# Performance work log

Hardware: AMD Instinct MI355X
Metric: run time of the kernel (lower is better)

Reference implementation:

```python
import jax, jax.numpy as jnp
import numpy as np

T, B, H, N2 = 4096, 2, 2048, 8  # seq_len, batch, embed_dim, ndim//2 complex modes


def setup_inputs() -> dict:
    key = jax.random.key(0)
    k1, k2, k3, k4, k5 = jax.random.split(key, 5)
    x = jax.random.normal(k1, (T, B, H), dtype=jnp.float32)
    D_param = jax.random.normal(k2, (H,), dtype=jnp.float32)
    # dt log-uniform in [1e-3, 1e-1] (standard S4D init)
    u = jax.random.uniform(k3, (H,), dtype=jnp.float32)
    log_dt = u * (jnp.log(0.1) - jnp.log(0.001)) + jnp.log(0.001)
    # S4D-Lin init: A = -1/2 + i*pi*n
    A_real_log = jnp.full((H, N2), jnp.log(0.5), dtype=jnp.float32)
    A_imag = jnp.broadcast_to(np.pi * jnp.arange(N2, dtype=jnp.float32), (H, N2))
    C_re = jax.random.normal(k4, (H, N2), dtype=jnp.float32)
    C_im = jax.random.normal(k5, (H, N2), dtype=jnp.float32)
    return {"x": x, "D_param": D_param, "log_dt": log_dt,
            "A_real_log": A_real_log, "A_imag": A_imag,
            "C_re": C_re, "C_im": C_im}


def _s4d_kernel(log_dt, A_real_log, A_imag, C_re, C_im, L):
    # Diagonal SSM (S4D, ZOH-style) convolution kernel, shape (H, L)
    dt = jnp.exp(log_dt)[:, None]                      # (H, 1)
    A = -jnp.exp(A_real_log) + 1j * A_imag             # (H, N2) complex64
    dtA = A * dt                                       # (H, N2)
    C = (C_re + 1j * C_im) * (jnp.exp(dtA) - 1.0) / A  # discretized C
    vander = jnp.exp(dtA[:, :, None] * jnp.arange(L))  # (H, N2, L)
    return 2.0 * jnp.einsum('hn,hnl->hl', C, vander).real


def reference(x, D_param, log_dt, A_real_log, A_imag, C_re, C_im):
    seq_len = x.shape[0]
    residual = x * D_param                     # (T, B, H)
    xb = jnp.transpose(x, (1, 2, 0))           # (B, H, T)
    k = _s4d_kernel(log_dt, A_real_log, A_imag, C_re, C_im, seq_len)  # (H, T)
    n = 2 * seq_len
    k_f = jnp.fft.rfft(k, n=n)                 # (H, T+1) complex
    x_f = jnp.fft.rfft(xb, n=n)                # (B, H, T+1)
    out = jnp.fft.irfft(x_f * k_f, n=n)[..., :seq_len]  # (B, H, T)
    return jnp.transpose(out, (2, 0, 1)) + residual      # (T, B, H)
```

## Files before the change

kernel.cpp:

```cpp
#include <hip/hip_runtime.h>

#define T_LEN 4096
#define B_SZ  2
#define H_SZ  2048
#define NM    8
#define BH    (B_SZ * H_SZ)


template <int LC>
__global__ void __launch_bounds__(256, 4)
k1_chunk_end(const float* __restrict__ x,
             const float* __restrict__ log_dt,
             const float* __restrict__ Arl,
             const float* __restrict__ Aimp,
             float2* __restrict__ states) {
    int g = blockIdx.x * blockDim.x + threadIdx.x;
    int h = g % H_SZ;
    int b = (g / H_SZ) % B_SZ;
    int c = g / BH;

    float dt = __expf(log_dt[h]);
    float wr[NM], wi[NM];
#pragma unroll
    for (int n = 0; n < NM; ++n) {
        float ar  = -__expf(Arl[h * NM + n]);
        float ai  = Aimp[h * NM + n];
        float er  = __expf(ar * dt);
        float ang = ai * dt;
        wr[n] = er * __cosf(ang);
        wi[n] = er * __sinf(ang);
    }

    float sr[NM], si[NM];
#pragma unroll
    for (int n = 0; n < NM; ++n) { sr[n] = 0.f; si[n] = 0.f; }

    const float* xp = x + (size_t)c * LC * BH + b * H_SZ + h;

    constexpr int BT = 8;
    float buf[BT], nxt[BT];
#pragma unroll
    for (int i = 0; i < BT; ++i) buf[i] = xp[(size_t)i * BH];

#pragma unroll
    for (int tb = 0; tb < LC / BT; ++tb) {
        if (tb + 1 < LC / BT) {
#pragma unroll
            for (int i = 0; i < BT; ++i)
                nxt[i] = xp[(size_t)((tb + 1) * BT + i) * BH];
        }
#pragma unroll
        for (int i = 0; i < BT; ++i) {
            float xv = buf[i];
#pragma unroll
            for (int n = 0; n < NM; ++n) {
                float nsr = fmaf(wr[n], sr[n], fmaf(-wi[n], si[n], xv));
                float nsi = fmaf(wr[n], si[n], wi[n] * sr[n]);
                sr[n] = nsr; si[n] = nsi;
            }
        }
#pragma unroll
        for (int i = 0; i < BT; ++i) buf[i] = nxt[i];
    }

    float2* st = states + (size_t)(c * B_SZ + b) * NM * H_SZ + h;
#pragma unroll
    for (int n = 0; n < NM; ++n) st[(size_t)n * H_SZ] = make_float2(sr[n], si[n]);
}

template <int CC, int LC>
__global__ void __launch_bounds__(256, 4)
k2_carry_scan(const float* __restrict__ log_dt,
              const float* __restrict__ Arl,
              const float* __restrict__ Aimp,
              float2* __restrict__ states) {
    int g = blockIdx.x * blockDim.x + threadIdx.x;
    int h = g % H_SZ;
    int n = (g / H_SZ) % NM;
    int b = g / (H_SZ * NM);

    float dt  = __expf(log_dt[h]);
    float Are = -__expf(Arl[h * NM + n]);
    float Aim = Aimp[h * NM + n];
    float er  = __expf(Are * dt * (float)LC);
    float ang = Aim * dt * (float)LC;
    float wr = er * __cosf(ang), wi = er * __sinf(ang);

    const size_t stride = (size_t)B_SZ * NM * H_SZ;
    float2* base = states + ((size_t)b * NM + n) * H_SZ + h;

    float cr = 0.f, ci = 0.f;
    constexpr int BT = 8;
    float2 buf[BT], nxt[BT];
#pragma unroll
    for (int i = 0; i < BT; ++i) buf[i] = base[(size_t)i * stride];

#pragma unroll
    for (int cb = 0; cb < CC / BT; ++cb) {
        if (cb + 1 < CC / BT) {
#pragma unroll
            for (int i = 0; i < BT; ++i)
                nxt[i] = base[(size_t)((cb + 1) * BT + i) * stride];
        }
#pragma unroll
        for (int i = 0; i < BT; ++i) {
            int c = cb * BT + i;
            base[(size_t)c * stride] = make_float2(cr, ci);
            float ncr = fmaf(wr, cr, fmaf(-wi, ci, buf[i].x));
            float nci = fmaf(wr, ci, fmaf(wi, cr, buf[i].y));
            cr = ncr; ci = nci;
        }
#pragma unroll
        for (int i = 0; i < BT; ++i) buf[i] = nxt[i];
    }
}

template <int LC>
__global__ void __launch_bounds__(256, 4)
k3_output(const float* __restrict__ x,
          const float* __restrict__ Dp,
          const float* __restrict__ log_dt,
          const float* __restrict__ Arl,
          const float* __restrict__ Aimp,
          const float* __restrict__ Crep,
          const float* __restrict__ Cimp,
          const float2* __restrict__ states,
          float* __restrict__ out) {
    int g = blockIdx.x * blockDim.x + threadIdx.x;
    int h = g % H_SZ;
    int b = (g / H_SZ) % B_SZ;
    int c = g / BH;

    float dt = __expf(log_dt[h]);
    float wr[NM], wi[NM], cdr[NM], cdi[NM];
#pragma unroll
    for (int n = 0; n < NM; ++n) {
        float ar  = -__expf(Arl[h * NM + n]);
        float ai  = Aimp[h * NM + n];
        float er  = __expf(ar * dt);
        float ang = ai * dt;
        float wrn = er * __cosf(ang);
        float win = er * __sinf(ang);
        wr[n] = wrn; wi[n] = win;
        float inv = 1.0f / (ar * ar + ai * ai);
        float tr = ((wrn - 1.f) * ar + win * ai) * inv;
        float ti = (win * ar - (wrn - 1.f) * ai) * inv;
        float Cre = Crep[h * NM + n], Cim = Cimp[h * NM + n];
        cdr[n] = Cre * tr - Cim * ti;
        cdi[n] = Cre * ti + Cim * tr;
    }

    const float2* st = states + (size_t)(c * B_SZ + b) * NM * H_SZ + h;
    float sr[NM], si[NM];
#pragma unroll
    for (int n = 0; n < NM; ++n) {
        float2 v = st[(size_t)n * H_SZ];
        sr[n] = v.x; si[n] = v.y;
    }

    float Dv = Dp[h];
    const float* xp = x + (size_t)c * LC * BH + b * H_SZ + h;
    float* op = out + (size_t)c * LC * BH + b * H_SZ + h;

    constexpr int BT = 8;
    float buf[BT], nxt[BT];
#pragma unroll
    for (int i = 0; i < BT; ++i) buf[i] = xp[(size_t)i * BH];

#pragma unroll
    for (int tb = 0; tb < LC / BT; ++tb) {
        if (tb + 1 < LC / BT) {
#pragma unroll
            for (int i = 0; i < BT; ++i)
                nxt[i] = xp[(size_t)((tb + 1) * BT + i) * BH];
        }
#pragma unroll
        for (int i = 0; i < BT; ++i) {
            float xv = buf[i];
            float y = 0.f;
#pragma unroll
            for (int n = 0; n < NM; ++n) {
                float nsr = fmaf(wr[n], sr[n], fmaf(-wi[n], si[n], xv));
                float nsi = fmaf(wr[n], si[n], wi[n] * sr[n]);
                sr[n] = nsr; si[n] = nsi;
                y = fmaf(cdr[n], nsr, y);
                y = fmaf(-cdi[n], nsi, y);
            }
            float ov = fmaf(Dv, xv, 2.0f * y);
            __builtin_nontemporal_store(ov, op + (size_t)(tb * BT + i) * BH);
        }
#pragma unroll
        for (int i = 0; i < BT; ++i) buf[i] = nxt[i];
    }
}

extern "C" void kernel_launch(void* const* d_in, const int* in_sizes, int n_in,
                              void* d_out, int out_size, void* d_ws, size_t ws_size,
                              hipStream_t stream) {
    const float* x      = (const float*)d_in[0];
    const float* Dp     = (const float*)d_in[1];
    const float* log_dt = (const float*)d_in[2];
    const float* Arl    = (const float*)d_in[3];
    const float* Aimp   = (const float*)d_in[4];
    const float* Cre    = (const float*)d_in[5];
    const float* Cim    = (const float*)d_in[6];
    float* out = (float*)d_out;
    float2* states = (float2*)d_ws;

    const size_t need64 = (size_t)64 * BH * NM * sizeof(float2);

    if (ws_size >= need64) {
        constexpr int C = 64, LC = T_LEN / 64;
        int total1 = C * BH;
        k1_chunk_end<LC><<<total1 / 256, 256, 0, stream>>>(x, log_dt, Arl, Aimp, states);
        int total2 = BH * NM;
        k2_carry_scan<C, LC><<<total2 / 256, 256, 0, stream>>>(log_dt, Arl, Aimp, states);
        k3_output<LC><<<total1 / 256, 256, 0, stream>>>(x, Dp, log_dt, Arl, Aimp,
                                                        Cre, Cim, states, out);
    } else {
        constexpr int C = 32, LC = T_LEN / 32;
        int total1 = C * BH;
        k1_chunk_end<LC><<<total1 / 256, 256, 0, stream>>>(x, log_dt, Arl, Aimp, states);
        int total2 = BH * NM;
        k2_carry_scan<C, LC><<<total2 / 256, 256, 0, stream>>>(log_dt, Arl, Aimp, states);
        k3_output<LC><<<total1 / 256, 256, 0, stream>>>(x, Dp, log_dt, Arl, Aimp,
                                                        Cre, Cim, states, out);
    }
}
```

Before: 151.7 us.

## Replace serial chunk-carry scan with LDS-transposed wavefront parallel scan

The carry-propagation kernel is rewritten so that each 64-lane wavefront does a Hillis-Steele complex linear-recurrence scan across the 64 chunks, using shuffles and an LDS transpose tile. The old version scanned the 64 chunks serially in a single thread per (b, n, h). This removes the serial dependency chain and gives coalesced loads of the chunk states. In exchange the scan does more total arithmetic, and the powers W^k come from repeated squaring, which can add rounding error. Separately, k1 now prefetches 16 timesteps instead of 8, and the fallback path for a small workspace is removed.

```diff
diff --git a/kernel.cpp b/kernel.cpp
--- a/kernel.cpp
+++ b/kernel.cpp
@@ -5,9 +5,11 @@
 #define H_SZ  2048
 #define NM    8
 #define BH    (B_SZ * H_SZ)
-
-
-template <int LC>
+#define C_CH  64
+#define LC    (T_LEN / C_CH)
+
+
+template <int BT>
 __global__ void __launch_bounds__(256, 4)
 k1_chunk_end(const float* __restrict__ x,
              const float* __restrict__ log_dt,
@@ -37,7 +39,6 @@
 
     const float* xp = x + (size_t)c * LC * BH + b * H_SZ + h;
 
-    constexpr int BT = 8;
     float buf[BT], nxt[BT];
 #pragma unroll
     for (int i = 0; i < BT; ++i) buf[i] = xp[(size_t)i * BH];
@@ -68,54 +69,75 @@
     for (int n = 0; n < NM; ++n) st[(size_t)n * H_SZ] = make_float2(sr[n], si[n]);
 }
 
-template <int CC, int LC>
 __global__ void __launch_bounds__(256, 4)
 k2_carry_scan(const float* __restrict__ log_dt,
               const float* __restrict__ Arl,
               const float* __restrict__ Aimp,
               float2* __restrict__ states) {
-    int g = blockIdx.x * blockDim.x + threadIdx.x;
-    int h = g % H_SZ;
-    int n = (g / H_SZ) % NM;
-    int b = g / (H_SZ * NM);
-
-    float dt  = __expf(log_dt[h]);
-    float Are = -__expf(Arl[h * NM + n]);
-    float Aim = Aimp[h * NM + n];
-    float er  = __expf(Are * dt * (float)LC);
-    float ang = Aim * dt * (float)LC;
-    float wr = er * __cosf(ang), wi = er * __sinf(ang);
-
-    const size_t stride = (size_t)B_SZ * NM * H_SZ;
-    float2* base = states + ((size_t)b * NM + n) * H_SZ + h;
-
-    float cr = 0.f, ci = 0.f;
-    constexpr int BT = 8;
-    float2 buf[BT], nxt[BT];
-#pragma unroll
-    for (int i = 0; i < BT; ++i) buf[i] = base[(size_t)i * stride];
-
-#pragma unroll
-    for (int cb = 0; cb < CC / BT; ++cb) {
-        if (cb + 1 < CC / BT) {
-#pragma unroll
-            for (int i = 0; i < BT; ++i)
-                nxt[i] = base[(size_t)((cb + 1) * BT + i) * stride];
-        }
-#pragma unroll
-        for (int i = 0; i < BT; ++i) {
-            int c = cb * BT + i;
-            base[(size_t)c * stride] = make_float2(cr, ci);
-            float ncr = fmaf(wr, cr, fmaf(-wi, ci, buf[i].x));
-            float nci = fmaf(wr, ci, fmaf(wi, cr, buf[i].y));
-            cr = ncr; ci = nci;
-        }
-#pragma unroll
-        for (int i = 0; i < BT; ++i) buf[i] = nxt[i];
-    }
-}
-
-template <int LC>
+    __shared__ float2 tile[C_CH][65];
+
+    int blk = blockIdx.x;
+    int ht = blk % (H_SZ / 64);
+    int n  = (blk / (H_SZ / 64)) % NM;
+    int b  = blk / ((H_SZ / 64) * NM);
+    int h0 = ht * 64;
+
+    int tid  = threadIdx.x;
+    int lane = tid & 63;
+    int wv   = tid >> 6;
+
+    const size_t cstride = (size_t)B_SZ * NM * H_SZ;
+    float2* base = states + ((size_t)b * NM + n) * H_SZ + h0;
+
+#pragma unroll
+    for (int i = 0; i < C_CH / 4; ++i) {
+        int c = i * 4 + wv;
+        tile[c][lane] = base[(size_t)c * cstride + lane];
+    }
+    __syncthreads();
+
+#pragma unroll
+    for (int ci = 0; ci < 16; ++ci) {
+        int hh = wv * 16 + ci;
+        int h  = h0 + hh;
+        float dt  = __expf(log_dt[h]);
+        float ar  = -__expf(Arl[h * NM + n]);
+        float ai  = Aimp[h * NM + n];
+        float er  = __expf(ar * dt * (float)LC);
+        float ang = ai * dt * (float)LC;
+        float Wr = er * __cosf(ang), Wi = er * __sinf(ang);
+
+        float2 v = tile[lane][hh];
+        float br = v.x, bi = v.y;
+
+        float Wkr = Wr, Wki = Wi;
+#pragma unroll
+        for (int k = 1; k < C_CH; k <<= 1) {
+            float pr = __shfl_up(br, k);
+            float pi = __shfl_up(bi, k);
+            if (lane >= k) {
+                br = fmaf(Wkr, pr, fmaf(-Wki, pi, br));
+                bi = fmaf(Wkr, pi, fmaf(Wki, pr, bi));
+            }
+            float nWr = Wkr * Wkr - Wki * Wki;
+            float nWi = 2.f * Wkr * Wki;
+            Wkr = nWr; Wki = nWi;
+        }
+        float er2 = __shfl_up(br, 1);
+        float ei2 = __shfl_up(bi, 1);
+        if (lane == 0) { er2 = 0.f; ei2 = 0.f; }
+        tile[lane][hh] = make_float2(er2, ei2);
+    }
+    __syncthreads();
+
+#pragma unroll
+    for (int i = 0; i < C_CH / 4; ++i) {
+        int c = i * 4 + wv;
+        base[(size_t)c * cstride + lane] = tile[c][lane];
+    }
+}
+
+template <int BT>
 __global__ void __launch_bounds__(256, 4)
 k3_output(const float* __restrict__ x,
           const float* __restrict__ Dp,
@@ -162,7 +184,6 @@
     const float* xp = x + (size_t)c * LC * BH + b * H_SZ + h;
     float* op = out + (size_t)c * LC * BH + b * H_SZ + h;
 
-    constexpr int BT = 8;
     float buf[BT], nxt[BT];
 #pragma unroll
     for (int i = 0; i < BT; ++i) buf[i] = xp[(size_t)i * BH];
@@ -207,23 +228,12 @@
     float* out = (float*)d_out;
     float2* states = (float2*)d_ws;
 
-    const size_t need64 = (size_t)64 * BH * NM * sizeof(float2);
-
-    if (ws_size >= need64) {
-        constexpr int C = 64, LC = T_LEN / 64;
-        int total1 = C * BH;
-        k1_chunk_end<LC><<<total1 / 256, 256, 0, stream>>>(x, log_dt, Arl, Aimp, states);
-        int total2 = BH * NM;
-        k2_carry_scan<C, LC><<<total2 / 256, 256, 0, stream>>>(log_dt, Arl, Aimp, states);
-        k3_output<LC><<<total1 / 256, 256, 0, stream>>>(x, Dp, log_dt, Arl, Aimp,
-                                                        Cre, Cim, states, out);
-    } else {
-        constexpr int C = 32, LC = T_LEN / 32;
-        int total1 = C * BH;
-        k1_chunk_end<LC><<<total1 / 256, 256, 0, stream>>>(x, log_dt, Arl, Aimp, states);
-        int total2 = BH * NM;
-        k2_carry_scan<C, LC><<<total2 / 256, 256, 0, stream>>>(log_dt, Arl, Aimp, states);
-        k3_output<LC><<<total1 / 256, 256, 0, stream>>>(x, Dp, log_dt, Arl, Aimp,
-                                                        Cre, Cim, states, out);
-    }
-}
+    int total1 = C_CH * BH;
+    k1_chunk_end<16><<<total1 / 256, 256, 0, stream>>>(x, log_dt, Arl, Aimp, states);
+
+    int blocks2 = B_SZ * NM * (H_SZ / 64);
+    k2_carry_scan<<<blocks2, 256, 0, stream>>>(log_dt, Arl, Aimp, states);
+
+    k3_output<8><<<total1 / 256, 256, 0, stream>>>(x, Dp, log_dt, Arl, Aimp,
+                                                   Cre, Cim, states, out);
+}
```

New measurement: 158.5 us. 1.05x slower.
